# Performance work log

Measured on AMD Instinct MI355X. Metric: run time of the kernel, lower is better.

## Reference

```python
import jax, jax.numpy as jnp
import numpy as np

N_HEAD = 16
N_FEAT = 1024
D_K = N_FEAT // N_HEAD
BATCH = 8
SEQ = 1024
LN_EPS = 1e-5
MIN_VAL = float(np.finfo(np.float32).min)


def setup_inputs() -> dict:
    key = jax.random.key(0)
    ks = jax.random.split(key, 8)
    s = 0.02  # small init scale for weights to keep activations sane
    return {
        "x": jax.random.normal(ks[0], (BATCH, SEQ, N_FEAT), jnp.float32),
        "pos_k": jax.random.normal(ks[1], (SEQ, SEQ, D_K), jnp.float32) * s,
        "mask": jnp.ones((BATCH, SEQ, SEQ), jnp.int32),
        "ln_scale": jnp.ones((N_FEAT,), jnp.float32),
        "ln_bias": jnp.zeros((N_FEAT,), jnp.float32),
        "wq": jax.random.normal(ks[2], (N_FEAT, N_FEAT), jnp.float32) * s,
        "bq": jnp.zeros((N_FEAT,), jnp.float32),
        "wk": jax.random.normal(ks[3], (N_FEAT, N_FEAT), jnp.float32) * s,
        "bk": jnp.zeros((N_FEAT,), jnp.float32),
        "wv": jax.random.normal(ks[4], (N_FEAT, N_FEAT), jnp.float32) * s,
        "bv": jnp.zeros((N_FEAT,), jnp.float32),
        "wo": jax.random.normal(ks[5], (N_FEAT, N_FEAT), jnp.float32) * s,
        "bo": jnp.zeros((N_FEAT,), jnp.float32),
    }


def reference(x, pos_k, mask, ln_scale, ln_bias, wq, bq, wk, bk, wv, bv, wo, bo):
    b, t, f = x.shape
    h, d = N_HEAD, D_K
    # LayerNorm over feature dim
    mu = jnp.mean(x, axis=-1, keepdims=True)
    var = jnp.mean((x - mu) ** 2, axis=-1, keepdims=True)
    xn = (x - mu) / jnp.sqrt(var + LN_EPS) * ln_scale + ln_bias
    # QKV projections (torch Linear: y = x @ W^T + b), split heads -> (b, h, t, d)
    q = (xn @ wq.T + bq).reshape(b, t, h, d).transpose(0, 2, 1, 3)
    k = (xn @ wk.T + bk).reshape(b, t, h, d).transpose(0, 2, 1, 3)
    v = (xn @ wv.T + bv).reshape(b, t, h, d).transpose(0, 2, 1, 3)
    # content score A and relative-position score B
    A = jnp.einsum("bhtd,bhsd->bhts", q, k)
    B = jnp.einsum("bhtd,tsd->bhts", q, pos_k)
    scores = (A + B) / jnp.sqrt(jnp.asarray(d, scores_dtype := x.dtype))
    m = (mask[:, None, :, :] == 0)  # (b, 1, t, s) broadcast over heads
    scores = jnp.where(m, MIN_VAL, scores)
    attn = jax.nn.softmax(scores, axis=-1)
    attn = jnp.where(m, 0.0, attn)
    out = jnp.einsum("bhts,bhsd->bhtd", attn, v)
    out = out.transpose(0, 2, 1, 3).reshape(b, t, h * d)
    return out @ wo.T + bo
```

## Files before the change

kernel.cpp:

```cpp
#include <hip/hip_runtime.h>
#include <hip/hip_bf16.h>

typedef unsigned short ushort_t;
typedef short short8 __attribute__((ext_vector_type(8)));
typedef unsigned short ushort8 __attribute__((ext_vector_type(8)));
typedef unsigned short ushortx4 __attribute__((ext_vector_type(4)));
typedef float fx4 __attribute__((ext_vector_type(4)));
typedef int ix4 __attribute__((ext_vector_type(4)));

#define MFMA(a, b, c) __builtin_amdgcn_mfma_f32_16x16x32_bf16((a), (b), (c), 0, 0, 0)

#define QSCALE 0.18033688011112042f

__device__ __forceinline__ ushort_t f2bf(float f) {
  __hip_bfloat16 h = __float2bfloat16(f);
  return *(ushort_t*)&h;
}
__device__ __forceinline__ float bf2f(ushort_t h) {
  union { unsigned u; float f; } c; c.u = ((unsigned)h) << 16;
  return c.f;
}
__device__ __forceinline__ void gload16(const ushort_t* g, ushort_t* l) {
  __builtin_amdgcn_global_load_lds((const __attribute__((address_space(1))) void*)g,
                                   (__attribute__((address_space(3))) void*)l, 16, 0, 0);
}

__global__ __launch_bounds__(256) void cvt4_kernel(const float* __restrict__ s0,
                                                   const float* __restrict__ s1,
                                                   const float* __restrict__ s2,
                                                   const float* __restrict__ s3,
                                                   ushort_t* __restrict__ d0,
                                                   ushort_t* __restrict__ d1,
                                                   ushort_t* __restrict__ d2,
                                                   ushort_t* __restrict__ d3) {
  int bi = blockIdx.x;
  const float* src = (bi < 1024) ? s0 : (bi < 2048) ? s1 : (bi < 3072) ? s2 : s3;
  ushort_t* dst = (bi < 1024) ? d0 : (bi < 2048) ? d1 : (bi < 3072) ? d2 : d3;
  int i = (bi & 1023) * 256 + threadIdx.x;
  fx4 v = *(const fx4*)&src[(size_t)i * 4];
  ushortx4 o;
#pragma unroll
  for (int j = 0; j < 4; ++j) o[j] = f2bf(v[j]);
  *(ushortx4*)&dst[(size_t)i * 4] = o;
}

__global__ __launch_bounds__(256) void ln_kernel(const float* __restrict__ x,
                                                 const float* __restrict__ sc,
                                                 const float* __restrict__ bi,
                                                 ushort_t* __restrict__ xn) {
  __shared__ float red[8];
  int row = blockIdx.x, tid = threadIdx.x;
  const float* xr = x + (size_t)row * 1024;
  fx4 v = *(const fx4*)&xr[tid * 4];
  float s = v[0] + v[1] + v[2] + v[3];
  float s2 = v[0] * v[0] + v[1] * v[1] + v[2] * v[2] + v[3] * v[3];
#pragma unroll
  for (int m = 32; m >= 1; m >>= 1) {
    s += __shfl_xor(s, m);
    s2 += __shfl_xor(s2, m);
  }
  int wave = tid >> 6;
  if ((tid & 63) == 0) { red[wave * 2] = s; red[wave * 2 + 1] = s2; }
  __syncthreads();
  s = red[0] + red[2] + red[4] + red[6];
  s2 = red[1] + red[3] + red[5] + red[7];
  float mu = s * (1.f / 1024.f);
  float var = s2 * (1.f / 1024.f) - mu * mu;
  float rs = rsqrtf(var + 1e-5f);
  fx4 scv = *(const fx4*)&sc[tid * 4];
  fx4 biv = *(const fx4*)&bi[tid * 4];
  ushortx4 o;
#pragma unroll
  for (int j = 0; j < 4; ++j) o[j] = f2bf((v[j] - mu) * rs * scv[j] + biv[j]);
  *(ushortx4*)&xn[(size_t)row * 1024 + tid * 4] = o;
}

__global__ __launch_bounds__(256) void maskpack_kernel(const int* __restrict__ mask,
                                                       unsigned* __restrict__ bits) {
  __shared__ unsigned char nib[256];
  int row = blockIdx.x, tid = threadIdx.x;
  ix4 m = *(const ix4*)&mask[(size_t)row * 1024 + tid * 4];
  nib[tid] = (unsigned char)((m[0] != 0 ? 1 : 0) | (m[1] != 0 ? 2 : 0) |
                             (m[2] != 0 ? 4 : 0) | (m[3] != 0 ? 8 : 0));
  __syncthreads();
  if (tid < 32) {
    unsigned w = 0;
#pragma unroll
    for (int j = 0; j < 8; ++j) w |= ((unsigned)nib[tid * 8 + j]) << (j * 4);
    bits[(size_t)row * 32 + tid] = w;
  }
}

template <int F32OUT>
__global__ __launch_bounds__(256) void gemm_bt(const ushort_t* __restrict__ A,
                                               const ushort_t* __restrict__ B,
                                               const float* __restrict__ bias, void* C,
                                               int M, int N, int K, float oscale) {
  __shared__ ushort_t lA[4096];
  __shared__ ushort_t lB[4096];
  int bm = blockIdx.y * 128, bn = blockIdx.x * 128;
  int tid = threadIdx.x;
  int wave = tid >> 6, lane = tid & 63;
  int wm = (wave >> 1) * 64, wn = (wave & 1) * 64;
  int l15 = lane & 15, lg = lane >> 4;
  int r0 = tid >> 2, c0 = (tid & 3) * 8;
  int g1 = 256 + tid, r1 = g1 >> 2, c1 = (g1 & 3) * 8;
  int lb0 = (wave * 64) * 8;
  int lb1 = (256 + wave * 64) * 8;
  fx4 acc[4][4] = {};
  for (int k0 = 0; k0 < K; k0 += 32) {
    __syncthreads();
    gload16(&A[(size_t)(bm + r0) * K + k0 + c0], &lA[lb0]);
    gload16(&A[(size_t)(bm + r1) * K + k0 + c1], &lA[lb1]);
    gload16(&B[(size_t)(bn + r0) * K + k0 + c0], &lB[lb0]);
    gload16(&B[(size_t)(bn + r1) * K + k0 + c1], &lB[lb1]);
    __syncthreads();
    short8 af[4], bf[4];
#pragma unroll
    for (int i = 0; i < 4; ++i) af[i] = *(const short8*)&lA[(wm + i * 16 + l15) * 32 + lg * 8];
#pragma unroll
    for (int i = 0; i < 4; ++i) bf[i] = *(const short8*)&lB[(wn + i * 16 + l15) * 32 + lg * 8];
#pragma unroll
    for (int i = 0; i < 4; ++i)
#pragma unroll
      for (int j = 0; j < 4; ++j) acc[i][j] = MFMA(af[i], bf[j], acc[i][j]);
  }
#pragma unroll
  for (int j = 0; j < 4; ++j) {
    int n = bn + wn + j * 16 + l15;
    float bv = bias[n];
#pragma unroll
    for (int i = 0; i < 4; ++i) {
      int mr = bm + wm + i * 16 + lg * 4;
#pragma unroll
      for (int r = 0; r < 4; ++r) {
        float val = (acc[i][j][r] + bv) * oscale;
        if (F32OUT)
          ((float*)C)[(size_t)(mr + r) * N + n] = val;
        else
          ((ushort_t*)C)[(size_t)(mr + r) * N + n] = f2bf(val);
      }
    }
  }
}

__device__ __forceinline__ void loadset(const float* base, int c, fx4* r) {
  const float* p = base + (size_t)c * 1024;
  r[0] = *(const fx4*)p;
  r[1] = *(const fx4*)(p + 4);
  r[2] = *(const fx4*)(p + 32);
  r[3] = *(const fx4*)(p + 36);
}
__device__ __forceinline__ void cvtset(const fx4* r, short8& f0, short8& f1) {
#pragma unroll
  for (int j = 0; j < 4; ++j) {
    f0[j] = (short)f2bf(r[0][j]); f0[j + 4] = (short)f2bf(r[1][j]);
    f1[j] = (short)f2bf(r[2][j]); f1[j + 4] = (short)f2bf(r[3][j]);
  }
}

__global__ __launch_bounds__(256, 3) void ball_kernel(const ushort_t* __restrict__ q,
                                                      const float* __restrict__ pos_k,
                                                      ushort_t* __restrict__ B_all) {
  __shared__ ushort_t lq[128 * 64];
  int t = blockIdx.y, sx = blockIdx.x;
  int tid = threadIdx.x, wave = tid >> 6, lane = tid & 63, l15 = lane & 15, lg = lane >> 4;
  const float* pk = pos_k + (size_t)t * 65536;
  int sw = sx * 512 + wave * 128;
  const float* base = pk + (size_t)(sw + l15) * 64 + lg * 8;

  fx4 raw[4][4];
#pragma unroll
  for (int c = 0; c < 4; ++c) loadset(base, c, raw[c]);

#pragma unroll
  for (int it = 0; it < 4; ++it) {
    int u = tid + it * 256;
    int row = u >> 3, cu = u & 7;
    ushort8 vv = *(const ushort8*)&q[((size_t)((row >> 4) * 1024 + t)) * 1024 + (row & 15) * 64 + cu * 8];
    *(ushort8*)&lq[(row * 128 + ((cu * 16) ^ ((row & 7) << 4))) >> 1] = vv;
  }
  __syncthreads();

  short8 af0[4], af1[4];
#pragma unroll
  for (int c = 0; c < 4; ++c) cvtset(raw[c], af0[c], af1[c]);

#pragma unroll
  for (int g = 0; g < 2; ++g) {
    if (g == 0) {
#pragma unroll
      for (int c = 0; c < 4; ++c) loadset(base, 4 + c, raw[c]);
    }
    __builtin_amdgcn_sched_barrier(0);
#pragma unroll
    for (int j = 0; j < 8; ++j) {
      int row_ = j * 16 + l15;
      int cb_ = (row_ & 7) << 4;
      short8 q0 = *(const short8*)&lq[(row_ * 128 + ((lg * 16) ^ cb_)) >> 1];
      short8 q1 = *(const short8*)&lq[(row_ * 128 + ((64 + lg * 16) ^ cb_)) >> 1];
      fx4 z = {};
      size_t rb = ((size_t)row_ << 20) + (size_t)t * 1024 + (size_t)(sw + g * 64);
#pragma unroll
      for (int c = 0; c < 4; ++c) {
        fx4 a = MFMA(af0[c], q0, z);
        a = MFMA(af1[c], q1, a);
        ushortx4 o;
#pragma unroll
        for (int r = 0; r < 4; ++r) o[r] = f2bf(a[r]);
        *(ushortx4*)&B_all[rb + c * 16 + lg * 4] = o;
      }
    }
    __builtin_amdgcn_sched_barrier(0);
    if (g == 0) {
#pragma unroll
      for (int c = 0; c < 4; ++c) cvtset(raw[c], af0[c], af1[c]);
    }
  }
}

__global__ __launch_bounds__(256) void attn_kernel(const ushort_t* __restrict__ q,
                                                   const ushort_t* __restrict__ k,
                                                   const ushort_t* __restrict__ v,
                                                   const ushort_t* __restrict__ B_all,
                                                   const unsigned* __restrict__ mbits,
                                                   ushort_t* __restrict__ out) {
  __shared__ ushort_t lK[64][72];
  __shared__ ushort_t lVt[64][72];
  __shared__ ushort_t lP[4][2][16][72];
  int bh = blockIdx.y, b = bh >> 4, h = bh & 15;
  int t0 = blockIdx.x * 128;
  int tid = threadIdx.x, wave = tid >> 6, lane = tid & 63, l15 = lane & 15, lg = lane >> 4;
  int twA = t0 + wave * 16, twB = twA + 64;
  short8 qfA[2], qfB[2];
#pragma unroll
  for (int ks = 0; ks < 2; ++ks) {
    qfA[ks] = *(const short8*)&q[((size_t)(b * 1024 + twA + l15)) * 1024 + h * 64 + ks * 32 + lg * 8];
    qfB[ks] = *(const short8*)&q[((size_t)(b * 1024 + twB + l15)) * 1024 + h * 64 + ks * 32 + lg * 8];
  }
  fx4 oA[4] = {}, oB[4] = {};
  float lsumA = 0.f, lsumB = 0.f;
  const unsigned* mrowA = &mbits[((size_t)b * 1024 + twA + l15) * 32];
  const unsigned* mrowB = &mbits[((size_t)b * 1024 + twB + l15) * 32];
  size_t ballA = ((size_t)bh * 1024 + twA + l15) * 1024;
  size_t ballB = ((size_t)bh * 1024 + twB + l15) * 1024;

  int rs = tid >> 3, c8g = tid & 7, c8 = c8g * 8;
  const ushort_t* kbase = &k[((size_t)(b * 1024) + rs) * 1024 + h * 64 + c8];
  const ushort_t* vbase = &v[((size_t)(b * 1024) + rs) * 1024 + h * 64 + c8];
  ushort8 kr0 = *(const ushort8*)(kbase);
  ushort8 kr1 = *(const ushort8*)(kbase + 32 * 1024);
  ushort8 vr0 = *(const ushort8*)(vbase);
  ushort8 vr1 = *(const ushort8*)(vbase + 32 * 1024);
  int vs0 = (rs + 8 * c8g) & 63;
  int vs1 = (rs + 32 + 8 * c8g) & 63;

  for (int s0 = 0; s0 < 1024; s0 += 64) {
    __syncthreads();
    *(ushort8*)&lK[rs][c8] = kr0;
    *(ushort8*)&lK[rs + 32][c8] = kr1;
#pragma unroll
    for (int j = 0; j < 8; ++j) {
      lVt[c8 + j][vs0] = vr0[j];
      lVt[c8 + j][vs1] = vr1[j];
    }
    __syncthreads();
    if (s0 + 64 < 1024) {
      size_t off = (size_t)(s0 + 64) * 1024;
      kr0 = *(const ushort8*)(kbase + off);
      kr1 = *(const ushort8*)(kbase + off + 32 * 1024);
      vr0 = *(const ushort8*)(vbase + off);
      vr1 = *(const ushort8*)(vbase + off + 32 * 1024);
    }
    __builtin_amdgcn_sched_barrier(0);
    ushortx4 b4A[4], b4B[4];
#pragma unroll
    for (int mf = 0; mf < 4; ++mf) {
      b4A[mf] = *(const ushortx4*)&B_all[ballA + s0 + mf * 16 + lg * 4];
      b4B[mf] = *(const ushortx4*)&B_all[ballB + s0 + mf * 16 + lg * 4];
    }
    uint2 mwA = *(const uint2*)&mrowA[s0 >> 5];
    uint2 mwB = *(const uint2*)&mrowB[s0 >> 5];
    unsigned long long wbA = ((unsigned long long)mwA.y << 32) | mwA.x;
    unsigned long long wbB = ((unsigned long long)mwB.y << 32) | mwB.x;
    __builtin_amdgcn_sched_barrier(0);
    float pA[16], pB[16];
#pragma unroll
    for (int mf = 0; mf < 4; ++mf) {
      short8 kf0 = *(const short8*)&lK[mf * 16 + l15][lg * 8];
      short8 kf1 = *(const short8*)&lK[mf * 16 + l15][32 + lg * 8];
      fx4 cA = {}, cB = {};
      cA = MFMA(kf0, qfA[0], cA);
      cA = MFMA(kf1, qfA[1], cA);
      cB = MFMA(kf0, qfB[0], cB);
      cB = MFMA(kf1, qfB[1], cB);
#pragma unroll
      for (int r = 0; r < 4; ++r) {
        pA[mf * 4 + r] = exp2f(cA[r] + bf2f(b4A[mf][r]));
        pB[mf * 4 + r] = exp2f(cB[r] + bf2f(b4B[mf][r]));
      }
    }
    if (!__all((wbA == ~0ull) && (wbB == ~0ull))) {
#pragma unroll
      for (int i = 0; i < 16; ++i) {
        int sl = (i >> 2) * 16 + lg * 4 + (i & 3);
        if (!((wbA >> sl) & 1ull)) pA[i] = 0.f;
        if (!((wbB >> sl) & 1ull)) pB[i] = 0.f;
      }
    }
    float psA = 0.f, psB = 0.f;
#pragma unroll
    for (int i = 0; i < 16; ++i) { psA += pA[i]; psB += pB[i]; }
    lsumA += psA;
    lsumB += psB;
#pragma unroll
    for (int mf = 0; mf < 4; ++mf) {
      ushortx4 pk4A, pk4B;
#pragma unroll
      for (int r = 0; r < 4; ++r) { pk4A[r] = f2bf(pA[mf * 4 + r]); pk4B[r] = f2bf(pB[mf * 4 + r]); }
      *(ushortx4*)&lP[wave][0][l15][mf * 16 + lg * 4] = pk4A;
      *(ushortx4*)&lP[wave][1][l15][mf * 16 + lg * 4] = pk4B;
    }
#pragma unroll
    for (int ks = 0; ks < 2; ++ks) {
      short8 pfA = *(const short8*)&lP[wave][0][l15][ks * 32 + lg * 8];
      short8 pfB = *(const short8*)&lP[wave][1][l15][ks * 32 + lg * 8];
#pragma unroll
      for (int nf = 0; nf < 4; ++nf) {
        int d_ = nf * 16 + l15;
        int sb_ = (ks * 32 + lg * 8 + 8 * (d_ >> 3)) & 63;
        short8 vf = *(const short8*)&lVt[d_][sb_];
        oA[nf] = MFMA(pfA, vf, oA[nf]);
        oB[nf] = MFMA(pfB, vf, oB[nf]);
      }
    }
  }
  lsumA += __shfl_xor(lsumA, 16);
  lsumA += __shfl_xor(lsumA, 32);
  lsumB += __shfl_xor(lsumB, 16);
  lsumB += __shfl_xor(lsumB, 32);
  float rlA = (lsumA > 0.f) ? 1.f / lsumA : 0.f;
  float rlB = (lsumB > 0.f) ? 1.f / lsumB : 0.f;
  float rwA[4], rwB[4];
#pragma unroll
  for (int r = 0; r < 4; ++r) {
    rwA[r] = __shfl(rlA, lg * 4 + r);
    rwB[r] = __shfl(rlB, lg * 4 + r);
  }
#pragma unroll
  for (int nf = 0; nf < 4; ++nf)
#pragma unroll
    for (int r = 0; r < 4; ++r) {
      out[((size_t)(b * 1024 + twA + lg * 4 + r)) * 1024 + h * 64 + nf * 16 + l15] =
          f2bf(oA[nf][r] * rwA[r]);
      out[((size_t)(b * 1024 + twB + lg * 4 + r)) * 1024 + h * 64 + nf * 16 + l15] =
          f2bf(oB[nf][r] * rwB[r]);
    }
}

extern "C" void kernel_launch(void* const* d_in, const int* in_sizes, int n_in, void* d_out,
                              int out_size, void* d_ws, size_t ws_size, hipStream_t stream) {
  (void)in_sizes; (void)n_in; (void)out_size; (void)ws_size;
  const float* x = (const float*)d_in[0];
  const float* pos_k = (const float*)d_in[1];
  const int* mask = (const int*)d_in[2];
  const float* ln_scale = (const float*)d_in[3];
  const float* ln_bias = (const float*)d_in[4];
  const float* wq = (const float*)d_in[5];
  const float* bq = (const float*)d_in[6];
  const float* wk = (const float*)d_in[7];
  const float* bk = (const float*)d_in[8];
  const float* wv = (const float*)d_in[9];
  const float* bv = (const float*)d_in[10];
  const float* wo = (const float*)d_in[11];
  const float* bo = (const float*)d_in[12];
  float* out = (float*)d_out;
  char* ws = (char*)d_ws;
  const size_t MB = 1ull << 20;
  ushort_t* xn = (ushort_t*)(ws + 0 * MB);
  ushort_t* qb = (ushort_t*)(ws + 16 * MB);
  ushort_t* kb = (ushort_t*)(ws + 32 * MB);
  ushort_t* vb = (ushort_t*)(ws + 48 * MB);
  ushort_t* ao = (ushort_t*)(ws + 64 * MB);
  ushort_t* wqb = (ushort_t*)(ws + 80 * MB);
  ushort_t* wkb = (ushort_t*)(ws + 82 * MB);
  ushort_t* wvb = (ushort_t*)(ws + 84 * MB);
  ushort_t* wob = (ushort_t*)(ws + 86 * MB);
  ushort_t* ball = (ushort_t*)(ws + 88 * MB);
  unsigned* mbits = (unsigned*)(ws + 0 * MB);

  cvt4_kernel<<<4096, 256, 0, stream>>>(wq, wk, wv, wo, wqb, wkb, wvb, wob);
  ln_kernel<<<8192, 256, 0, stream>>>(x, ln_scale, ln_bias, xn);
  dim3 gg(8, 64);
  gemm_bt<0><<<gg, 256, 0, stream>>>(xn, wqb, bq, qb, 8192, 1024, 1024, QSCALE);
  gemm_bt<0><<<gg, 256, 0, stream>>>(xn, wkb, bk, kb, 8192, 1024, 1024, 1.f);
  gemm_bt<0><<<gg, 256, 0, stream>>>(xn, wvb, bv, vb, 8192, 1024, 1024, 1.f);
  maskpack_kernel<<<8192, 256, 0, stream>>>(mask, mbits);
  ball_kernel<<<dim3(2, 1024), 256, 0, stream>>>(qb, pos_k, ball);
  attn_kernel<<<dim3(8, 128), 256, 0, stream>>>(qb, kb, vb, ball, mbits, ao);
  gemm_bt<1><<<gg, 256, 0, stream>>>(ao, wob, bo, out, 8192, 1024, 1024, 1.f);
}
```

Baseline: 415.4 us.

## Fuse QKV projections into one GEMM, split ball work finer, prefetch bias tiles

```diff
diff --git a/kernel.cpp b/kernel.cpp
--- a/kernel.cpp
+++ b/kernel.cpp
@@ -94,8 +94,10 @@
 template <int F32OUT>
 __global__ __launch_bounds__(256) void gemm_bt(const ushort_t* __restrict__ A,
                                                const ushort_t* __restrict__ B,
-                                               const float* __restrict__ bias, void* C,
-                                               int M, int N, int K, float oscale) {
+                                               const float* __restrict__ b0,
+                                               const float* __restrict__ b1,
+                                               const float* __restrict__ b2, void* C,
+                                               int M, int N, int K, float os0, float os1) {
   __shared__ ushort_t lA[4096];
   __shared__ ushort_t lB[4096];
   int bm = blockIdx.y * 128, bn = blockIdx.x * 128;
@@ -128,13 +130,15 @@
 #pragma unroll
   for (int j = 0; j < 4; ++j) {
     int n = bn + wn + j * 16 + l15;
-    float bv = bias[n];
+    const float* bp = (n < 1024) ? b0 : (n < 2048) ? b1 : b2;
+    float bv = bp[n & 1023];
+    float sc = (n < 1024) ? os0 : os1;
 #pragma unroll
     for (int i = 0; i < 4; ++i) {
       int mr = bm + wm + i * 16 + lg * 4;
 #pragma unroll
       for (int r = 0; r < 4; ++r) {
-        float val = (acc[i][j][r] + bv) * oscale;
+        float val = (acc[i][j][r] + bv) * sc;
         if (F32OUT)
           ((float*)C)[(size_t)(mr + r) * N + n] = val;
         else
@@ -159,14 +163,14 @@
   }
 }
 
-__global__ __launch_bounds__(256, 3) void ball_kernel(const ushort_t* __restrict__ q,
+__global__ __launch_bounds__(256, 3) void ball_kernel(const ushort_t* __restrict__ qkv,
                                                       const float* __restrict__ pos_k,
                                                       ushort_t* __restrict__ B_all) {
   __shared__ ushort_t lq[128 * 64];
   int t = blockIdx.y, sx = blockIdx.x;
   int tid = threadIdx.x, wave = tid >> 6, lane = tid & 63, l15 = lane & 15, lg = lane >> 4;
   const float* pk = pos_k + (size_t)t * 65536;
-  int sw = sx * 512 + wave * 128;
+  int sw = sx * 256 + wave * 64;
   const float* base = pk + (size_t)(sw + l15) * 64 + lg * 8;
 
   fx4 raw[4][4];
@@ -177,7 +181,7 @@
   for (int it = 0; it < 4; ++it) {
     int u = tid + it * 256;
     int row = u >> 3, cu = u & 7;
-    ushort8 vv = *(const ushort8*)&q[((size_t)((row >> 4) * 1024 + t)) * 1024 + (row & 15) * 64 + cu * 8];
+    ushort8 vv = *(const ushort8*)&qkv[((size_t)((row >> 4) * 1024 + t)) * 3072 + (row & 15) * 64 + cu * 8];
     *(ushort8*)&lq[(row * 128 + ((cu * 16) ^ ((row & 7) << 4))) >> 1] = vv;
   }
   __syncthreads();
@@ -187,41 +191,26 @@
   for (int c = 0; c < 4; ++c) cvtset(raw[c], af0[c], af1[c]);
 
 #pragma unroll
-  for (int g = 0; g < 2; ++g) {
-    if (g == 0) {
-#pragma unroll
-      for (int c = 0; c < 4; ++c) loadset(base, 4 + c, raw[c]);
-    }
-    __builtin_amdgcn_sched_barrier(0);
-#pragma unroll
-    for (int j = 0; j < 8; ++j) {
-      int row_ = j * 16 + l15;
-      int cb_ = (row_ & 7) << 4;
-      short8 q0 = *(const short8*)&lq[(row_ * 128 + ((lg * 16) ^ cb_)) >> 1];
-      short8 q1 = *(const short8*)&lq[(row_ * 128 + ((64 + lg * 16) ^ cb_)) >> 1];
-      fx4 z = {};
-      size_t rb = ((size_t)row_ << 20) + (size_t)t * 1024 + (size_t)(sw + g * 64);
-#pragma unroll
-      for (int c = 0; c < 4; ++c) {
-        fx4 a = MFMA(af0[c], q0, z);
-        a = MFMA(af1[c], q1, a);
-        ushortx4 o;
-#pragma unroll
-        for (int r = 0; r < 4; ++r) o[r] = f2bf(a[r]);
-        *(ushortx4*)&B_all[rb + c * 16 + lg * 4] = o;
-      }
-    }
-    __builtin_amdgcn_sched_barrier(0);
-    if (g == 0) {
-#pragma unroll
-      for (int c = 0; c < 4; ++c) cvtset(raw[c], af0[c], af1[c]);
-    }
-  }
-}
-
-__global__ __launch_bounds__(256) void attn_kernel(const ushort_t* __restrict__ q,
-                                                   const ushort_t* __restrict__ k,
-                                                   const ushort_t* __restrict__ v,
+  for (int j = 0; j < 8; ++j) {
+    int row_ = j * 16 + l15;
+    int cb_ = (row_ & 7) << 4;
+    short8 q0 = *(const short8*)&lq[(row_ * 128 + ((lg * 16) ^ cb_)) >> 1];
+    short8 q1 = *(const short8*)&lq[(row_ * 128 + ((64 + lg * 16) ^ cb_)) >> 1];
+    fx4 z = {};
+    size_t rb = ((size_t)row_ << 20) + (size_t)t * 1024 + (size_t)sw;
+#pragma unroll
+    for (int c = 0; c < 4; ++c) {
+      fx4 a = MFMA(af0[c], q0, z);
+      a = MFMA(af1[c], q1, a);
+      ushortx4 o;
+#pragma unroll
+      for (int r = 0; r < 4; ++r) o[r] = f2bf(a[r]);
+      *(ushortx4*)&B_all[rb + c * 16 + lg * 4] = o;
+    }
+  }
+}
+
+__global__ __launch_bounds__(256) void attn_kernel(const ushort_t* __restrict__ qkv,
                                                    const ushort_t* __restrict__ B_all,
                                                    const unsigned* __restrict__ mbits,
                                                    ushort_t* __restrict__ out) {
@@ -235,8 +224,8 @@
   short8 qfA[2], qfB[2];
 #pragma unroll
   for (int ks = 0; ks < 2; ++ks) {
-    qfA[ks] = *(const short8*)&q[((size_t)(b * 1024 + twA + l15)) * 1024 + h * 64 + ks * 32 + lg * 8];
-    qfB[ks] = *(const short8*)&q[((size_t)(b * 1024 + twB + l15)) * 1024 + h * 64 + ks * 32 + lg * 8];
+    qfA[ks] = *(const short8*)&qkv[((size_t)(b * 1024 + twA + l15)) * 3072 + h * 64 + ks * 32 + lg * 8];
+    qfB[ks] = *(const short8*)&qkv[((size_t)(b * 1024 + twB + l15)) * 3072 + h * 64 + ks * 32 + lg * 8];
   }
   fx4 oA[4] = {}, oB[4] = {};
   float lsumA = 0.f, lsumB = 0.f;
@@ -246,14 +235,23 @@
   size_t ballB = ((size_t)bh * 1024 + twB + l15) * 1024;
 
   int rs = tid >> 3, c8g = tid & 7, c8 = c8g * 8;
-  const ushort_t* kbase = &k[((size_t)(b * 1024) + rs) * 1024 + h * 64 + c8];
-  const ushort_t* vbase = &v[((size_t)(b * 1024) + rs) * 1024 + h * 64 + c8];
+  const ushort_t* kbase = &qkv[((size_t)(b * 1024) + rs) * 3072 + 1024 + h * 64 + c8];
+  const ushort_t* vbase = &qkv[((size_t)(b * 1024) + rs) * 3072 + 2048 + h * 64 + c8];
   ushort8 kr0 = *(const ushort8*)(kbase);
-  ushort8 kr1 = *(const ushort8*)(kbase + 32 * 1024);
+  ushort8 kr1 = *(const ushort8*)(kbase + 32 * 3072);
   ushort8 vr0 = *(const ushort8*)(vbase);
-  ushort8 vr1 = *(const ushort8*)(vbase + 32 * 1024);
+  ushort8 vr1 = *(const ushort8*)(vbase + 32 * 3072);
   int vs0 = (rs + 8 * c8g) & 63;
   int vs1 = (rs + 32 + 8 * c8g) & 63;
+
+  ushortx4 n4A[4], n4B[4];
+#pragma unroll
+  for (int mf = 0; mf < 4; ++mf) {
+    n4A[mf] = *(const ushortx4*)&B_all[ballA + mf * 16 + lg * 4];
+    n4B[mf] = *(const ushortx4*)&B_all[ballB + mf * 16 + lg * 4];
+  }
+  uint2 nmA = *(const uint2*)&mrowA[0];
+  uint2 nmB = *(const uint2*)&mrowB[0];
 
   for (int s0 = 0; s0 < 1024; s0 += 64) {
     __syncthreads();
@@ -266,24 +264,15 @@
     }
     __syncthreads();
     if (s0 + 64 < 1024) {
-      size_t off = (size_t)(s0 + 64) * 1024;
+      size_t off = (size_t)(s0 + 64) * 3072;
       kr0 = *(const ushort8*)(kbase + off);
-      kr1 = *(const ushort8*)(kbase + off + 32 * 1024);
+      kr1 = *(const ushort8*)(kbase + off + 32 * 3072);
       vr0 = *(const ushort8*)(vbase + off);
-      vr1 = *(const ushort8*)(vbase + off + 32 * 1024);
+      vr1 = *(const ushort8*)(vbase + off + 32 * 3072);
     }
     __builtin_amdgcn_sched_barrier(0);
-    ushortx4 b4A[4], b4B[4];
-#pragma unroll
-    for (int mf = 0; mf < 4; ++mf) {
-      b4A[mf] = *(const ushortx4*)&B_all[ballA + s0 + mf * 16 + lg * 4];
-      b4B[mf] = *(const ushortx4*)&B_all[ballB + s0 + mf * 16 + lg * 4];
-    }
-    uint2 mwA = *(const uint2*)&mrowA[s0 >> 5];
-    uint2 mwB = *(const uint2*)&mrowB[s0 >> 5];
-    unsigned long long wbA = ((unsigned long long)mwA.y << 32) | mwA.x;
-    unsigned long long wbB = ((unsigned long long)mwB.y << 32) | mwB.x;
-    __builtin_amdgcn_sched_barrier(0);
+    unsigned long long wbA = ((unsigned long long)nmA.y << 32) | nmA.x;
+    unsigned long long wbB = ((unsigned long long)nmB.y << 32) | nmB.x;
     float pA[16], pB[16];
 #pragma unroll
     for (int mf = 0; mf < 4; ++mf) {
@@ -296,8 +285,8 @@
       cB = MFMA(kf1, qfB[1], cB);
 #pragma unroll
       for (int r = 0; r < 4; ++r) {
-        pA[mf * 4 + r] = exp2f(cA[r] + bf2f(b4A[mf][r]));
-        pB[mf * 4 + r] = exp2f(cB[r] + bf2f(b4B[mf][r]));
+        pA[mf * 4 + r] = exp2f(cA[r] + bf2f(n4A[mf][r]));
+        pB[mf * 4 + r] = exp2f(cB[r] + bf2f(n4B[mf][r]));
       }
     }
     if (!__all((wbA == ~0ull) && (wbB == ~0ull))) {
@@ -308,6 +297,16 @@
         if (!((wbB >> sl) & 1ull)) pB[i] = 0.f;
       }
     }
+    if (s0 + 64 < 1024) {
+#pragma unroll
+      for (int mf = 0; mf < 4; ++mf) {
+        n4A[mf] = *(const ushortx4*)&B_all[ballA + s0 + 64 + mf * 16 + lg * 4];
+        n4B[mf] = *(const ushortx4*)&B_all[ballB + s0 + 64 + mf * 16 + lg * 4];
+      }
+      nmA = *(const uint2*)&mrowA[(s0 + 64) >> 5];
+      nmB = *(const uint2*)&mrowB[(s0 + 64) >> 5];
+    }
+    __builtin_amdgcn_sched_barrier(0);
     float psA = 0.f, psB = 0.f;
 #pragma unroll
     for (int i = 0; i < 16; ++i) { psA += pA[i]; psB += pB[i]; }
@@ -378,9 +377,7 @@
   char* ws = (char*)d_ws;
   const size_t MB = 1ull << 20;
   ushort_t* xn = (ushort_t*)(ws + 0 * MB);
-  ushort_t* qb = (ushort_t*)(ws + 16 * MB);
-  ushort_t* kb = (ushort_t*)(ws + 32 * MB);
-  ushort_t* vb = (ushort_t*)(ws + 48 * MB);
+  ushort_t* qkv = (ushort_t*)(ws + 16 * MB);
   ushort_t* ao = (ushort_t*)(ws + 64 * MB);
   ushort_t* wqb = (ushort_t*)(ws + 80 * MB);
   ushort_t* wkb = (ushort_t*)(ws + 82 * MB);
@@ -391,12 +388,11 @@
 
   cvt4_kernel<<<4096, 256, 0, stream>>>(wq, wk, wv, wo, wqb, wkb, wvb, wob);
   ln_kernel<<<8192, 256, 0, stream>>>(x, ln_scale, ln_bias, xn);
-  dim3 gg(8, 64);
-  gemm_bt<0><<<gg, 256, 0, stream>>>(xn, wqb, bq, qb, 8192, 1024, 1024, QSCALE);
-  gemm_bt<0><<<gg, 256, 0, stream>>>(xn, wkb, bk, kb, 8192, 1024, 1024, 1.f);
-  gemm_bt<0><<<gg, 256, 0, stream>>>(xn, wvb, bv, vb, 8192, 1024, 1024, 1.f);
+  gemm_bt<0><<<dim3(24, 64), 256, 0, stream>>>(xn, wqb, bq, bk, bv, qkv, 8192, 3072, 1024,
+                                               QSCALE, 1.f);
   maskpack_kernel<<<8192, 256, 0, stream>>>(mask, mbits);
-  ball_kernel<<<dim3(2, 1024), 256, 0, stream>>>(qb, pos_k, ball);
-  attn_kernel<<<dim3(8, 128), 256, 0, stream>>>(qb, kb, vb, ball, mbits, ao);
-  gemm_bt<1><<<gg, 256, 0, stream>>>(ao, wob, bo, out, 8192, 1024, 1024, 1.f);
-}
+  ball_kernel<<<dim3(4, 1024), 256, 0, stream>>>(qkv, pos_k, ball);
+  attn_kernel<<<dim3(8, 128), 256, 0, stream>>>(qkv, ball, mbits, ao);
+  gemm_bt<1><<<dim3(8, 64), 256, 0, stream>>>(ao, wob, bo, bo, bo, out, 8192, 1024, 1024,
+                                              1.f, 1.f);
+}
```

Result: faster. 372.6 us (-10.3%).
